# Optimization experiments

Hardware: AMD Instinct MI355X
Metric: run time of the kernel (lower is better)

The kernel has to match this reference:

```python
import jax, jax.numpy as jnp
import numpy as np

H = 16  # num_heads


def setup_inputs() -> dict:
    key = jax.random.key(0)
    ks = jax.random.split(key, 8)
    B, N, C = 16, 4096, 512
    hd = C // H
    sc = lambda k, shape: jax.random.normal(k, shape, jnp.float32) * 0.02
    return {
        "x": jax.random.normal(ks[0], (B, N, C), jnp.float32),
        "Wqkv": sc(ks[1], (C, 3 * C)),
        "bqkv": sc(ks[2], (3 * C,)),
        "pos_enc": jnp.zeros((1, N, C), jnp.float32),
        "dwc_w": sc(ks[3], (hd, 1, 5, 5)),  # OIHW, depthwise: groups = hd
        "dwc_b": sc(ks[4], (hd,)),
        "Wproj": sc(ks[5], (C, C)),
        "bproj": sc(ks[6], (C,)),
    }


def reference(x, Wqkv, bqkv, pos_enc, dwc_w, dwc_b, Wproj, bproj):
    B, N, C = x.shape
    hd = C // H
    # qkv projection
    qkv = x @ Wqkv + bqkv                       # (B, N, 3C)
    q, k, v = jnp.split(qkv, 3, axis=-1)
    k = k + pos_enc
    q = jax.nn.relu(q)
    k = jax.nn.relu(k)

    def heads(t):  # (B, N, C) -> (B*H, N, hd), fp32 as in the torch autocast-off block
        return t.reshape(B, N, H, hd).transpose(0, 2, 1, 3).reshape(B * H, N, hd).astype(jnp.float32)

    q, k, v = heads(q), heads(k), heads(v)
    # normalization z_i = 1 / (q_i . sum_j k_j + eps)
    z = 1.0 / (jnp.einsum('bic,bc->bi', q, k.sum(axis=1)) + 1e-6)   # (B*H, N)
    # kv-first path: i*j*(c+d) > c*d*(i+j) for N=4096, hd=32
    kv = jnp.einsum('bjc,bjd->bcd', k, v)                           # (B*H, hd, hd)
    out = jnp.einsum('bic,bcd->bid', q, kv) * z[..., None]          # (B*H, N, hd)
    # depthwise 5x5 conv on v reshaped to a square feature map
    w = int(N ** 0.5)
    fm = v.transpose(0, 2, 1).reshape(B * H, hd, w, w)
    fm = jax.lax.conv_general_dilated(
        fm, dwc_w, window_strides=(1, 1), padding=[(2, 2), (2, 2)],
        dimension_numbers=('NCHW', 'OIHW', 'NCHW'), feature_group_count=hd)
    fm = fm + dwc_b[None, :, None, None]
    fm = fm.reshape(B * H, hd, N).transpose(0, 2, 1)
    out = out + fm
    # merge heads and project
    out = out.reshape(B, H, N, hd).transpose(0, 2, 1, 3).reshape(B, N, C)
    return out @ Wproj + bproj
```

## Files before the change

kernel.cpp:

```cpp
#include <hip/hip_runtime.h>
#include <stdint.h>

typedef short bf16x8 __attribute__((ext_vector_type(8)));
typedef float f32x4 __attribute__((ext_vector_type(4)));
typedef unsigned short u16x8 __attribute__((ext_vector_type(8)));

__device__ __forceinline__ unsigned short f2bf(float f){
  uint32_t u = __builtin_bit_cast(uint32_t, f);
  u += 0x7FFFu + ((u >> 16) & 1u);
  return (unsigned short)(u >> 16);
}
__device__ __forceinline__ float bf2f(unsigned short h){
  uint32_t u = ((uint32_t)h) << 16;
  return __builtin_bit_cast(float, u);
}
__device__ __forceinline__ float bflo(uint32_t dw){
  return __builtin_bit_cast(float, dw << 16);
}
__device__ __forceinline__ float bfhi(uint32_t dw){
  return __builtin_bit_cast(float, dw & 0xffff0000u);
}

__device__ __forceinline__ void gload_lds16(const void* g, void* l){
  __builtin_amdgcn_global_load_lds(
      (const __attribute__((address_space(1))) uint32_t*)(g),
      (__attribute__((address_space(3))) uint32_t*)(l),
      16, 0, 0);
}

__global__ __launch_bounds__(256) void convert_x_k(const float* __restrict__ x,
                                                   unsigned short* __restrict__ xb){
  size_t i = (size_t)blockIdx.x * 256 + threadIdx.x;
  const float4* p = (const float4*)x + i * 2;
  float4 a = p[0], b = p[1];
  u16x8 o;
  o[0] = f2bf(a.x); o[1] = f2bf(a.y); o[2] = f2bf(a.z); o[3] = f2bf(a.w);
  o[4] = f2bf(b.x); o[5] = f2bf(b.y); o[6] = f2bf(b.z); o[7] = f2bf(b.w);
  *(u16x8*)(xb + i * 8) = o;
}

__global__ __launch_bounds__(256) void transpose_w_k(const float* __restrict__ Wqkv,
                                                     const float* __restrict__ Wproj,
                                                     unsigned short* __restrict__ Wqkvt,
                                                     unsigned short* __restrict__ Wprojt){
  __shared__ unsigned short t[64][68];
  int bid = blockIdx.x;
  const float* src; unsigned short* dst; int c0, j0, sstride, dstride;
  if (bid < 192){
    src = Wqkv;  dst = Wqkvt;  sstride = 1536; dstride = 512;
    c0 = (bid / 24) * 64;  j0 = (bid % 24) * 64;
  } else {
    int e = bid - 192;
    src = Wproj; dst = Wprojt; sstride = 512;  dstride = 512;
    c0 = (e >> 3) * 64;    j0 = (e & 7) * 64;
  }
  int tid = threadIdx.x;
  int rl = tid >> 6;
  int cl = tid & 63;
  #pragma unroll
  for (int i = 0; i < 16; ++i){
    int cr = i * 4 + rl;
    t[cl][cr] = f2bf(src[(size_t)(c0 + cr) * sstride + j0 + cl]);
  }
  __syncthreads();
  #pragma unroll
  for (int i = 0; i < 16; ++i){
    int jr = i * 4 + rl;
    dst[(size_t)(j0 + jr) * dstride + c0 + cl] = t[jr][cl];
  }
}

__global__ __launch_bounds__(512, 2) void gemm_qkv(
    const unsigned short* __restrict__ A,
    const unsigned short* __restrict__ Bt,
    const float* __restrict__ bias,
    const float* __restrict__ pos_enc,
    unsigned short* __restrict__ oq,
    unsigned short* __restrict__ ok,
    unsigned short* __restrict__ ov,
    int NTN)
{
  __shared__ unsigned short As[256 * 64];
  __shared__ unsigned short Bs[128 * 64];
  int tid = threadIdx.x, lane = tid & 63, wid = tid >> 6;
  int nwg = gridDim.x;
  int b0 = blockIdx.x;
  int cpx = nwg >> 3;
  int swz = (b0 & 7) * cpx + (b0 >> 3);
  int tm = swz / NTN, tn = swz - tm * NTN;
  int row0 = tm << 8, col0 = tn << 7;
  int wr = wid >> 1, wc = wid & 1;

  f32x4 acc[4][4];
  #pragma unroll
  for (int m = 0; m < 4; ++m)
    #pragma unroll
    for (int n = 0; n < 4; ++n)
      acc[m][n] = (f32x4){0.f, 0.f, 0.f, 0.f};

  for (int kt = 0; kt < 8; ++kt){
    int k0 = kt * 64;
    #pragma unroll
    for (int it = 0; it < 4; ++it){
      int c = it * 512 + tid;
      int r = c >> 3;
      int scs = ((c & 7) ^ (r & 7)) * 8;
      gload_lds16(A + (size_t)(row0 + r) * 512 + k0 + scs, &As[c * 8]);
    }
    #pragma unroll
    for (int it = 0; it < 2; ++it){
      int c = it * 512 + tid;
      int r = c >> 3;
      int scs = ((c & 7) ^ (r & 7)) * 8;
      gload_lds16(Bt + (size_t)(col0 + r) * 512 + k0 + scs, &Bs[c * 8]);
    }
    __syncthreads();
    #pragma unroll
    for (int kk = 0; kk < 2; ++kk){
      bf16x8 af[4], bfr[4];
      int kcs = ((kk * 4 + (lane >> 4)) ^ (lane & 7)) * 8;
      #pragma unroll
      for (int m = 0; m < 4; ++m)
        af[m] = *(const bf16x8*)&As[(wr * 64 + m * 16 + (lane & 15)) * 64 + kcs];
      #pragma unroll
      for (int n = 0; n < 4; ++n)
        bfr[n] = *(const bf16x8*)&Bs[(wc * 64 + n * 16 + (lane & 15)) * 64 + kcs];
      #pragma unroll
      for (int m = 0; m < 4; ++m)
        #pragma unroll
        for (int n = 0; n < 4; ++n)
          acc[m][n] = __builtin_amdgcn_mfma_f32_16x16x32_bf16(af[m], bfr[n], acc[m][n], 0, 0, 0);
    }
    __syncthreads();
  }

  int part = col0 >> 9;
  int ccb = (col0 & 511) + wc * 64;
  unsigned short* scr = &As[wid * 2048];
  #pragma unroll
  for (int mh = 0; mh < 2; ++mh){
    #pragma unroll
    for (int mm = 0; mm < 2; ++mm){
      int m = mh * 2 + mm;
      #pragma unroll
      for (int n = 0; n < 4; ++n){
        #pragma unroll
        for (int r = 0; r < 4; ++r){
          int lrow = mm * 16 + (lane >> 4) * 4 + r;
          int lcol = n * 16 + (lane & 15);
          float val = acc[m][n][r] + bias[col0 + wc * 64 + lcol];
          if (part == 0) val = fmaxf(val, 0.f);
          int pch = (lcol >> 3) ^ ((lrow >> 2) & 3);
          scr[lrow * 64 + pch * 8 + (lcol & 7)] = f2bf(val);
        }
      }
    }
    #pragma unroll
    for (int i = 0; i < 4; ++i){
      int idx = i * 64 + lane;
      int r2 = idx >> 3, c2 = idx & 7;
      int pch = c2 ^ ((r2 >> 2) & 3);
      u16x8 vals = *(const u16x8*)&scr[r2 * 64 + pch * 8];
      int grow = row0 + wr * 64 + mh * 32 + r2;
      int bb = grow >> 12, nn = grow & 4095;
      int cc = ccb + c2 * 8;
      int h = cc >> 5, d = cc & 31;
      size_t dst = ((size_t)((bb << 4) + h) * 4096 + nn) * 32 + d;
      if (part == 1){
        const float4* pe = (const float4*)(pos_enc + (size_t)nn * 512 + cc);
        float4 p0 = pe[0], p1 = pe[1];
        u16x8 o;
        o[0] = f2bf(fmaxf(bf2f(vals[0]) + p0.x, 0.f));
        o[1] = f2bf(fmaxf(bf2f(vals[1]) + p0.y, 0.f));
        o[2] = f2bf(fmaxf(bf2f(vals[2]) + p0.z, 0.f));
        o[3] = f2bf(fmaxf(bf2f(vals[3]) + p0.w, 0.f));
        o[4] = f2bf(fmaxf(bf2f(vals[4]) + p1.x, 0.f));
        o[5] = f2bf(fmaxf(bf2f(vals[5]) + p1.y, 0.f));
        o[6] = f2bf(fmaxf(bf2f(vals[6]) + p1.z, 0.f));
        o[7] = f2bf(fmaxf(bf2f(vals[7]) + p1.w, 0.f));
        *(u16x8*)(ok + dst) = o;
      } else if (part == 0){
        *(u16x8*)(oq + dst) = vals;
      } else {
        *(u16x8*)(ov + dst) = vals;
      }
    }
  }
}

__global__ __launch_bounds__(512, 1) void gemm_proj(
    const unsigned short* __restrict__ A,
    const unsigned short* __restrict__ Bt,
    const float* __restrict__ bias,
    float* __restrict__ op,
    int NTN)
{
  __shared__ unsigned short As[2][256 * 64];
  __shared__ unsigned short Bs[2][256 * 64];
  int tid = threadIdx.x, lane = tid & 63, wid = tid >> 6;
  int nwg = gridDim.x;
  int b0 = blockIdx.x;
  int cpx = nwg >> 3;
  int swz = (b0 & 7) * cpx + (b0 >> 3);
  int tm = swz / NTN, tn = swz - tm * NTN;
  int row0 = tm << 8, col0 = tn << 8;
  int wrow = wid >> 2, wcol = wid & 3;

  f32x4 acc[8][4];
  #pragma unroll
  for (int m = 0; m < 8; ++m)
    #pragma unroll
    for (int n = 0; n < 4; ++n)
      acc[m][n] = (f32x4){0.f, 0.f, 0.f, 0.f};

  auto STAGE = [&](int buf, int kt){
    int k0 = kt * 64;
    #pragma unroll
    for (int it = 0; it < 4; ++it){
      int c = it * 512 + tid;
      int r = c >> 3;
      int scs = ((c & 7) ^ (r & 7)) * 8;
      gload_lds16(A + (size_t)(row0 + r) * 512 + k0 + scs, &As[buf][c * 8]);
    }
    #pragma unroll
    for (int it = 0; it < 4; ++it){
      int c = it * 512 + tid;
      int r = c >> 3;
      int scs = ((c & 7) ^ (r & 7)) * 8;
      gload_lds16(Bt + (size_t)(col0 + r) * 512 + k0 + scs, &Bs[buf][c * 8]);
    }
  };
  auto COMPUTE = [&](int buf){
    bf16x8 bfr[4][2];
    #pragma unroll
    for (int kk = 0; kk < 2; ++kk){
      int kcs = ((kk * 4 + (lane >> 4)) ^ (lane & 7)) * 8;
      #pragma unroll
      for (int n = 0; n < 4; ++n)
        bfr[n][kk] = *(const bf16x8*)&Bs[buf][(wcol * 64 + n * 16 + (lane & 15)) * 64 + kcs];
    }
    __builtin_amdgcn_s_setprio(1);
    #pragma unroll
    for (int kk = 0; kk < 2; ++kk){
      int kcs = ((kk * 4 + (lane >> 4)) ^ (lane & 7)) * 8;
      #pragma unroll
      for (int m = 0; m < 8; ++m){
        bf16x8 af = *(const bf16x8*)&As[buf][(wrow * 128 + m * 16 + (lane & 15)) * 64 + kcs];
        #pragma unroll
        for (int n = 0; n < 4; ++n)
          acc[m][n] = __builtin_amdgcn_mfma_f32_16x16x32_bf16(af, bfr[n][kk], acc[m][n], 0, 0, 0);
      }
    }
    __builtin_amdgcn_s_setprio(0);
  };

  STAGE(0, 0);
  STAGE(1, 1);
  #pragma unroll
  for (int t = 0; t < 8; ++t){
    if (t < 7) asm volatile("s_waitcnt vmcnt(8)" ::: "memory");
    else       asm volatile("s_waitcnt vmcnt(0)" ::: "memory");
    __builtin_amdgcn_s_barrier();
    __builtin_amdgcn_sched_barrier(0);
    COMPUTE(t & 1);
    asm volatile("" ::: "memory");
    __builtin_amdgcn_s_barrier();
    if (t + 2 < 8) STAGE(t & 1, t + 2);
  }

  #pragma unroll
  for (int m = 0; m < 8; ++m){
    #pragma unroll
    for (int n = 0; n < 4; ++n){
      #pragma unroll
      for (int r = 0; r < 4; ++r){
        int rrow = row0 + wrow * 128 + m * 16 + (lane >> 4) * 4 + r;
        int ccol = col0 + wcol * 64 + n * 16 + (lane & 15);
        op[(size_t)rrow * 512 + ccol] = acc[m][n][r] + bias[ccol];
      }
    }
  }
}

__global__ __launch_bounds__(256) void kv_k(const unsigned short* __restrict__ kbuf,
                                            const unsigned short* __restrict__ vbuf,
                                            float* __restrict__ kvb,
                                            float* __restrict__ ksb,
                                            uint32_t* __restrict__ vp){
  int bh  = blockIdx.x >> 2;
  int seg = blockIdx.x & 3;
  __shared__ float ks[64][36];
  __shared__ float vs[64][36];
  __shared__ float red[4][64][16];
  __shared__ float ksred[4][8][4];
  int tid = threadIdx.x;
  int g = tid >> 6, gi = tid & 63;
  int c0 = (gi >> 3) * 4, d0 = (gi & 7) * 4;
  float acc[4][4] = {};
  float ksacc[4] = {0.f, 0.f, 0.f, 0.f};
  const unsigned short* kb = kbuf + (size_t)bh * 4096 * 32 + (size_t)seg * 1024 * 32;
  const unsigned short* vb = vbuf + (size_t)bh * 4096 * 32 + (size_t)seg * 1024 * 32;
  uint32_t* vpb = vp + (size_t)bh * 65536 + seg * 1024;
  int er = tid >> 2;
  int ec = (tid & 3) * 8;
  for (int t = 0; t < 16; ++t){
    __syncthreads();
    u16x8 kk8 = *(const u16x8*)(kb + ((size_t)t * 64 + er) * 32 + ec);
    u16x8 vv8 = *(const u16x8*)(vb + ((size_t)t * 64 + er) * 32 + ec);
    #pragma unroll
    for (int i = 0; i < 8; ++i){ ks[er][ec + i] = bf2f(kk8[i]); vs[er][ec + i] = bf2f(vv8[i]); }
    __syncthreads();
    #pragma unroll
    for (int i = 0; i < 4; ++i){
      int idx = i * 256 + tid;
      int pr = idx >> 6, tok = idx & 63;
      uint32_t pk = ((uint32_t)f2bf(vs[tok][pr * 2 + 1]) << 16)
                  |  (uint32_t)f2bf(vs[tok][pr * 2]);
      vpb[pr * 4096 + t * 64 + tok] = pk;
    }
    for (int nn = g; nn < 64; nn += 4){
      f32x4 k4 = *(const f32x4*)&ks[nn][c0];
      f32x4 v4 = *(const f32x4*)&vs[nn][d0];
      #pragma unroll
      for (int i = 0; i < 4; ++i)
        #pragma unroll
        for (int j = 0; j < 4; ++j)
          acc[i][j] += k4[i] * v4[j];
      if ((gi & 7) == 0){
        #pragma unroll
        for (int i = 0; i < 4; ++i) ksacc[i] += k4[i];
      }
    }
  }
  __syncthreads();
  #pragma unroll
  for (int i = 0; i < 4; ++i)
    #pragma unroll
    for (int j = 0; j < 4; ++j)
      red[g][gi][i * 4 + j] = acc[i][j];
  if ((gi & 7) == 0){
    #pragma unroll
    for (int i = 0; i < 4; ++i) ksred[g][gi >> 3][i] = ksacc[i];
  }
  __syncthreads();
  for (int s = tid; s < 1024; s += 256){
    int gi2 = s >> 4, e = s & 15;
    float sum = red[0][gi2][e] + red[1][gi2][e] + red[2][gi2][e] + red[3][gi2][e];
    int c = (gi2 >> 3) * 4 + (e >> 2), d = (gi2 & 7) * 4 + (e & 3);
    atomicAdd(&kvb[bh * 1024 + c * 32 + d], sum);
  }
  if (tid < 32){
    float s = ksred[0][tid >> 2][tid & 3] + ksred[1][tid >> 2][tid & 3]
            + ksred[2][tid >> 2][tid & 3] + ksred[3][tid >> 2][tid & 3];
    atomicAdd(&ksb[bh * 32 + tid], s);
  }
}

__global__ __launch_bounds__(256, 2) void attn_k3(
    const unsigned short* __restrict__ qbuf,
    const uint32_t* __restrict__ vp,
    const float* __restrict__ kvb,
    const float* __restrict__ ksb,
    const float* __restrict__ dwc_w,
    const float* __restrict__ dwc_b,
    unsigned short* __restrict__ attn)
{
  int band = blockIdx.x;
  int bh   = blockIdx.y;
  int tid = threadIdx.x, lane = tid & 63, w = tid >> 6;
  __shared__ uint32_t outs32[1024][18];
  unsigned short* outs = (unsigned short*)outs32;
  __shared__ float zs[1024];
  __shared__ float ksum_s[32];

  const unsigned short* qb = qbuf + (size_t)bh * 4096 * 32 + (size_t)band * 1024 * 32;
  const uint32_t* vpb = vp + (size_t)bh * 65536;

  if (tid < 32) ksum_s[tid] = ksb[bh * 32 + tid];
  __syncthreads();

  for (int p = 0; p < 4; ++p){
    int t = p * 256 + tid;
    float zd = 0.f;
    #pragma unroll
    for (int pp = 0; pp < 4; ++pp){
      u16x8 qq = *(const u16x8*)(qb + (size_t)t * 32 + pp * 8);
      #pragma unroll
      for (int i = 0; i < 8; ++i) zd += bf2f(qq[i]) * ksum_s[pp * 8 + i];
    }
    zs[t] = 1.f / (zd + 1e-6f);
  }

  bf16x8 bfr[2];
  #pragma unroll
  for (int nc = 0; nc < 2; ++nc){
    bf16x8 t8;
    #pragma unroll
    for (int j = 0; j < 8; ++j){
      int c = (lane >> 4) * 8 + j;
      int d = nc * 16 + (lane & 15);
      t8[j] = (short)f2bf(kvb[bh * 1024 + c * 32 + d]);
    }
    bfr[nc] = t8;
  }
  __syncthreads();

  for (int p = 0; p < 4; ++p){
    f32x4 acc[4][2];
    #pragma unroll
    for (int m = 0; m < 4; ++m){ acc[m][0] = (f32x4){0.f,0.f,0.f,0.f}; acc[m][1] = (f32x4){0.f,0.f,0.f,0.f}; }
    #pragma unroll
    for (int m = 0; m < 4; ++m){
      int row = p * 256 + w * 64 + m * 16 + (lane & 15);
      bf16x8 af = *(const bf16x8*)(qb + (size_t)row * 32 + (lane >> 4) * 8);
      acc[m][0] = __builtin_amdgcn_mfma_f32_16x16x32_bf16(af, bfr[0], acc[m][0], 0, 0, 0);
      acc[m][1] = __builtin_amdgcn_mfma_f32_16x16x32_bf16(af, bfr[1], acc[m][1], 0, 0, 0);
    }
    #pragma unroll
    for (int m = 0; m < 4; ++m)
      #pragma unroll
      for (int nc = 0; nc < 2; ++nc)
        #pragma unroll
        for (int r = 0; r < 4; ++r){
          int lrow = p * 256 + w * 64 + m * 16 + (lane >> 4) * 4 + r;
          int col = nc * 16 + (lane & 15);
          outs[lrow * 36 + col] = f2bf(acc[m][nc][r] * zs[lrow]);
        }
  }
  __syncthreads();

  int x = lane;
  int y0 = band * 16;
  int xm2 = lane - 2, xm1 = lane - 1, xp1 = lane + 1, xp2 = lane + 2;

  for (int pair = 0; pair < 4; ++pair){
    int dbase = w * 8 + pair * 2;
    int pr = w * 4 + pair;
    float w0[25], w1[25];
    #pragma unroll
    for (int j = 0; j < 25; ++j){
      w0[j] = dwc_w[dbase * 25 + j];
      w1[j] = dwc_w[(dbase + 1) * 25 + j];
    }
    float cb0 = dwc_b[dbase], cb1 = dwc_b[dbase + 1];

    uint32_t rowd[20];
    #pragma unroll
    for (int il = 0; il < 20; ++il){
      int yi = y0 - 2 + il;
      rowd[il] = (yi >= 0 && yi < 64)
        ? vpb[pr * 4096 + yi * 64 + x] : 0u;
    }

    float a0[5], a1[5];
    #pragma unroll
    for (int il = 0; il < 20; ++il){
      uint32_t d0 = rowd[il];
      uint32_t dm2 = (uint32_t)__shfl((int)d0, xm2); if (lane < 2)  dm2 = 0;
      uint32_t dm1 = (uint32_t)__shfl((int)d0, xm1); if (lane < 1)  dm1 = 0;
      uint32_t dp1 = (uint32_t)__shfl((int)d0, xp1); if (lane > 62) dp1 = 0;
      uint32_t dp2 = (uint32_t)__shfl((int)d0, xp2); if (lane > 61) dp2 = 0;
      float f0[5], f1[5];
      f0[0] = bflo(dm2); f1[0] = bfhi(dm2);
      f0[1] = bflo(dm1); f1[1] = bfhi(dm1);
      f0[2] = bflo(d0);  f1[2] = bfhi(d0);
      f0[3] = bflo(dp1); f1[3] = bfhi(dp1);
      f0[4] = bflo(dp2); f1[4] = bfhi(dp2);
      #pragma unroll
      for (int ky = 0; ky < 5; ++ky){
        int ol = il - ky;
        if (ol < 0 || ol > 15) continue;
        int s = ol % 5;
        if (ky == 0){
          a0[s] = w0[0] * f0[0];
          a1[s] = w1[0] * f1[0];
          #pragma unroll
          for (int kx = 1; kx < 5; ++kx){
            a0[s] += w0[kx] * f0[kx];
            a1[s] += w1[kx] * f1[kx];
          }
        } else {
          #pragma unroll
          for (int kx = 0; kx < 5; ++kx){
            a0[s] += w0[ky * 5 + kx] * f0[kx];
            a1[s] += w1[ky * 5 + kx] * f1[kx];
          }
        }
      }
      if (il >= 4){
        int ol = il - 4;
        int s = ol % 5;
        int ltok = ol * 64 + x;
        uint32_t ov = outs32[ltok][pr];
        float o0 = bflo(ov) + a0[s] + cb0;
        float o1 = bfhi(ov) + a1[s] + cb1;
        outs32[ltok][pr] = ((uint32_t)f2bf(o1) << 16) | (uint32_t)f2bf(o0);
      }
    }
  }
  __syncthreads();

  int b = bh >> 4, h = bh & 15;
  size_t gbase = ((size_t)b * 4096 + (size_t)band * 1024) * 512 + h * 32;
  #pragma unroll
  for (int it = 0; it < 32; ++it){
    int idx = it * 256 + tid;
    int token = idx >> 3, sub = idx & 7;
    uint2 vv = *(const uint2*)&outs32[token][sub * 2];
    *(uint2*)(attn + gbase + (size_t)token * 512 + sub * 4) = vv;
  }
}

extern "C" void kernel_launch(void* const* d_in, const int* in_sizes, int n_in,
                              void* d_out, int out_size, void* d_ws, size_t ws_size,
                              hipStream_t stream) {
  const float* x       = (const float*)d_in[0];
  const float* Wqkv    = (const float*)d_in[1];
  const float* bqkv    = (const float*)d_in[2];
  const float* pos_enc = (const float*)d_in[3];
  const float* dwc_w   = (const float*)d_in[4];
  const float* dwc_b   = (const float*)d_in[5];
  const float* Wproj   = (const float*)d_in[6];
  const float* bproj   = (const float*)d_in[7];
  float* out = (float*)d_out;
  char* ws = (char*)d_ws;

  const size_t off_xb    = 0;
  const size_t off_wqkvt = 67108864;
  const size_t off_wprojt= 68681728;
  const size_t off_q     = 69206016;
  const size_t off_k     = 136314880;
  const size_t off_v     = 203423744;
  const size_t off_kv    = 270532608;
  const size_t off_ksum  = 271581184;
  const size_t needed    = 271613952;
  if (ws_size < needed) return;

  unsigned short* xb     = (unsigned short*)(ws + off_xb);
  unsigned short* wqkvt  = (unsigned short*)(ws + off_wqkvt);
  unsigned short* wprojt = (unsigned short*)(ws + off_wprojt);
  unsigned short* qb     = (unsigned short*)(ws + off_q);
  unsigned short* kb     = (unsigned short*)(ws + off_k);
  unsigned short* vb     = (unsigned short*)(ws + off_v);
  float* kvb = (float*)(ws + off_kv);
  float* ksb = (float*)(ws + off_ksum);
  unsigned short* attn = kb;
  uint32_t* vp = (uint32_t*)(ws + off_xb);

  convert_x_k<<<16384, 256, 0, stream>>>(x, xb);
  transpose_w_k<<<256, 256, 0, stream>>>(Wqkv, Wproj, wqkvt, wprojt);
  gemm_qkv<<<3072, 512, 0, stream>>>(xb, wqkvt, bqkv, pos_enc, qb, kb, vb, 12);
  (void)hipMemsetAsync(kvb, 0, (size_t)(256 * 1024 + 256 * 32) * sizeof(float), stream);
  kv_k<<<1024, 256, 0, stream>>>(kb, vb, kvb, ksb, vp);
  attn_k3<<<dim3(4, 256), 256, 0, stream>>>(qb, vp, kvb, ksb, dwc_w, dwc_b, attn);
  gemm_proj<<<512, 512, 0, stream>>>(attn, wprojt, bproj, out, 2);
}
```

Measured before the change: 390.0 us.

## Compute KV outer product and key sums with MFMA on transposed swizzled LDS

```diff
diff --git a/kernel.cpp b/kernel.cpp
--- a/kernel.cpp
+++ b/kernel.cpp
@@ -289,70 +289,96 @@
                                             uint32_t* __restrict__ vp){
   int bh  = blockIdx.x >> 2;
   int seg = blockIdx.x & 3;
-  __shared__ float ks[64][36];
-  __shared__ float vs[64][36];
-  __shared__ float red[4][64][16];
-  __shared__ float ksred[4][8][4];
-  int tid = threadIdx.x;
-  int g = tid >> 6, gi = tid & 63;
-  int c0 = (gi >> 3) * 4, d0 = (gi & 7) * 4;
-  float acc[4][4] = {};
-  float ksacc[4] = {0.f, 0.f, 0.f, 0.f};
-  const unsigned short* kb = kbuf + (size_t)bh * 4096 * 32 + (size_t)seg * 1024 * 32;
-  const unsigned short* vb = vbuf + (size_t)bh * 4096 * 32 + (size_t)seg * 1024 * 32;
+  __shared__ unsigned short ksT[32 * 64];
+  __shared__ unsigned short vsT[32 * 64];
+  __shared__ float red[4][1024];
+  __shared__ float red2[4][32];
+  int tid = threadIdx.x, lane = tid & 63, w = tid >> 6;
+  const unsigned short* kb = kbuf + (size_t)bh * 131072 + (size_t)seg * 32768;
+  const unsigned short* vb = vbuf + (size_t)bh * 131072 + (size_t)seg * 32768;
   uint32_t* vpb = vp + (size_t)bh * 65536 + seg * 1024;
-  int er = tid >> 2;
-  int ec = (tid & 3) * 8;
+
+  f32x4 acc00 = (f32x4){0,0,0,0}, acc01 = (f32x4){0,0,0,0};
+  f32x4 acc10 = (f32x4){0,0,0,0}, acc11 = (f32x4){0,0,0,0};
+  f32x4 ksa0  = (f32x4){0,0,0,0}, ksa1  = (f32x4){0,0,0,0};
+  bf16x8 ones;
+  #pragma unroll
+  for (int j = 0; j < 8; ++j) ones[j] = (short)0x3F80;
+
+  int tok = tid >> 2;
+  int ec  = (tid & 3) * 8;
+
   for (int t = 0; t < 16; ++t){
     __syncthreads();
-    u16x8 kk8 = *(const u16x8*)(kb + ((size_t)t * 64 + er) * 32 + ec);
-    u16x8 vv8 = *(const u16x8*)(vb + ((size_t)t * 64 + er) * 32 + ec);
-    #pragma unroll
-    for (int i = 0; i < 8; ++i){ ks[er][ec + i] = bf2f(kk8[i]); vs[er][ec + i] = bf2f(vv8[i]); }
+    u16x8 kk8 = *(const u16x8*)(kb + ((size_t)t * 64 + tok) * 32 + ec);
+    u16x8 vv8 = *(const u16x8*)(vb + ((size_t)t * 64 + tok) * 32 + ec);
+    #pragma unroll
+    for (int j = 0; j < 8; ++j){
+      int row = ec + j;
+      int sw = (row + (row >> 3)) & 7;
+      int col = ((((tok >> 3) ^ sw) << 3) | (tok & 7));
+      ksT[row * 64 + col] = kk8[j];
+      vsT[row * 64 + col] = vv8[j];
+    }
     __syncthreads();
     #pragma unroll
     for (int i = 0; i < 4; ++i){
       int idx = i * 256 + tid;
-      int pr = idx >> 6, tok = idx & 63;
-      uint32_t pk = ((uint32_t)f2bf(vs[tok][pr * 2 + 1]) << 16)
-                  |  (uint32_t)f2bf(vs[tok][pr * 2]);
-      vpb[pr * 4096 + t * 64 + tok] = pk;
-    }
-    for (int nn = g; nn < 64; nn += 4){
-      f32x4 k4 = *(const f32x4*)&ks[nn][c0];
-      f32x4 v4 = *(const f32x4*)&vs[nn][d0];
-      #pragma unroll
-      for (int i = 0; i < 4; ++i)
-        #pragma unroll
-        for (int j = 0; j < 4; ++j)
-          acc[i][j] += k4[i] * v4[j];
-      if ((gi & 7) == 0){
-        #pragma unroll
-        for (int i = 0; i < 4; ++i) ksacc[i] += k4[i];
-      }
-    }
-  }
-  __syncthreads();
-  #pragma unroll
-  for (int i = 0; i < 4; ++i)
-    #pragma unroll
-    for (int j = 0; j < 4; ++j)
-      red[g][gi][i * 4 + j] = acc[i][j];
-  if ((gi & 7) == 0){
-    #pragma unroll
-    for (int i = 0; i < 4; ++i) ksred[g][gi >> 3][i] = ksacc[i];
+      int pr = idx >> 6, tk = idx & 63;
+      int r0 = pr * 2, r1 = r0 + 1;
+      int sw0 = (r0 + (r0 >> 3)) & 7;
+      int sw1 = (r1 + (r1 >> 3)) & 7;
+      uint32_t lo = ksT[0];
+      lo = vsT[r0 * 64 + ((((tk >> 3) ^ sw0) << 3) | (tk & 7))];
+      uint32_t hi = vsT[r1 * 64 + ((((tk >> 3) ^ sw1) << 3) | (tk & 7))];
+      vpb[pr * 4096 + t * 64 + tk] = lo | (hi << 16);
+    }
+    if ((t & 3) == w){
+      #pragma unroll
+      for (int kk = 0; kk < 2; ++kk){
+        int kc = kk * 4 + (lane >> 4);
+        int r0 = lane & 15, r1 = 16 + (lane & 15);
+        int sw0 = (r0 + (r0 >> 3)) & 7;
+        int sw1 = (r1 + (r1 >> 3)) & 7;
+        bf16x8 a0 = *(const bf16x8*)&ksT[r0 * 64 + ((kc ^ sw0) << 3)];
+        bf16x8 a1 = *(const bf16x8*)&ksT[r1 * 64 + ((kc ^ sw1) << 3)];
+        bf16x8 b0 = *(const bf16x8*)&vsT[r0 * 64 + ((kc ^ sw0) << 3)];
+        bf16x8 b1 = *(const bf16x8*)&vsT[r1 * 64 + ((kc ^ sw1) << 3)];
+        acc00 = __builtin_amdgcn_mfma_f32_16x16x32_bf16(a0, b0, acc00, 0, 0, 0);
+        acc01 = __builtin_amdgcn_mfma_f32_16x16x32_bf16(a0, b1, acc01, 0, 0, 0);
+        acc10 = __builtin_amdgcn_mfma_f32_16x16x32_bf16(a1, b0, acc10, 0, 0, 0);
+        acc11 = __builtin_amdgcn_mfma_f32_16x16x32_bf16(a1, b1, acc11, 0, 0, 0);
+        ksa0  = __builtin_amdgcn_mfma_f32_16x16x32_bf16(a0, ones, ksa0, 0, 0, 0);
+        ksa1  = __builtin_amdgcn_mfma_f32_16x16x32_bf16(a1, ones, ksa1, 0, 0, 0);
+      }
+    }
+  }
+  __syncthreads();
+  {
+    int q = lane >> 4, c16 = lane & 15;
+    #pragma unroll
+    for (int r = 0; r < 4; ++r){
+      red[w][(q * 4 + r) * 32 + c16]           = acc00[r];
+      red[w][(q * 4 + r) * 32 + 16 + c16]      = acc01[r];
+      red[w][(16 + q * 4 + r) * 32 + c16]      = acc10[r];
+      red[w][(16 + q * 4 + r) * 32 + 16 + c16] = acc11[r];
+    }
+    if (c16 == 0){
+      #pragma unroll
+      for (int r = 0; r < 4; ++r){
+        red2[w][q * 4 + r]      = ksa0[r];
+        red2[w][16 + q * 4 + r] = ksa1[r];
+      }
+    }
   }
   __syncthreads();
   for (int s = tid; s < 1024; s += 256){
-    int gi2 = s >> 4, e = s & 15;
-    float sum = red[0][gi2][e] + red[1][gi2][e] + red[2][gi2][e] + red[3][gi2][e];
-    int c = (gi2 >> 3) * 4 + (e >> 2), d = (gi2 & 7) * 4 + (e & 3);
-    atomicAdd(&kvb[bh * 1024 + c * 32 + d], sum);
+    float sum = red[0][s] + red[1][s] + red[2][s] + red[3][s];
+    atomicAdd(&kvb[bh * 1024 + s], sum);
   }
   if (tid < 32){
-    float s = ksred[0][tid >> 2][tid & 3] + ksred[1][tid >> 2][tid & 3]
-            + ksred[2][tid >> 2][tid & 3] + ksred[3][tid >> 2][tid & 3];
-    atomicAdd(&ksb[bh * 32 + tid], s);
+    atomicAdd(&ksb[bh * 32 + tid],
+              red2[0][tid] + red2[1][tid] + red2[2][tid] + red2[3][tid]);
   }
 }
 
```

New measurement: 366.8 us. 1.06x faster.
